# Kernel optimization log

Measured on AMD Instinct MI355X. Metric: run time of the kernel, lower is better.

Reference implementation:

```python
import jax, jax.numpy as jnp
import numpy as np
from jax import lax

BATCH, C, HH, WW = 4, 3, 512, 512


def _dark_min(x, patch):
    # min over channels, reflect-pad, min over patch x patch window (torch unfold+min)
    pad = (patch - 1) // 2
    m = jnp.min(x, axis=1, keepdims=True)                      # [B,1,H,W]
    m = jnp.pad(m, ((0, 0), (0, 0), (pad, pad), (pad, pad)), mode='reflect')
    return lax.reduce_window(m, jnp.array(jnp.inf, m.dtype), lax.min,
                             (1, 1, patch, patch), (1, 1, 1, 1), 'VALID')


def _soft_thresh(x, lam):
    return jnp.sign(x) * jnp.maximum(jnp.abs(x) - lam, 0.0)


def _conv3x3(x, w):
    return lax.conv_general_dilated(x, w, (1, 1), 'SAME',
                                    dimension_numbers=('NCHW', 'OIHW', 'NCHW'))


def setup_inputs() -> dict:
    key = jax.random.key(0)
    names = ['I', 't_p', 'B_p', 'B', 't', 'J', 'G', 'H', 'P', 'Q', 'u', 'v', 'X', 'Y']
    keys = jax.random.split(key, len(names) + 2)
    inp = {n: jax.random.uniform(keys[i], (BATCH, C, HH, WW), dtype=jnp.float32)
           for i, n in enumerate(names)}
    for g in ['gamma_1', 'gamma_2', 'gamma_3', 'gamma_4', 'gamma_5']:
        inp[g] = jnp.array([3.001], dtype=jnp.float32)
    inp['t1d_w'] = jax.random.normal(keys[-2], (1, 3, 1, 1), dtype=jnp.float32) * 0.3
    inp['hnet_w'] = jax.random.normal(keys[-1], (3, 3, 3, 3), dtype=jnp.float32) * 0.1
    inp['patch_size'] = 35
    return inp


def _forward(I, t_p, B_p, B, t, J, G, H, P, Q, u, v, X, Y,
             gamma_1, gamma_2, gamma_3, gamma_4, gamma_5, t1d_w, hnet_w, patch_size):
    lam1, lam2, lam3, lam4, lam5 = 1.0, 0.7, 0.3, 1.0, 1.0

    # ---- get_mean_value + mapping_index (vectorized over batch) ----
    mean = jnp.mean(J, axis=(2, 3))                 # [B,3]
    idx = jnp.argsort(mean, axis=1)                 # ascending, like torch.sort
    ms = jnp.take_along_axis(mean, idx, axis=1)     # sorted means
    gather = lambda k: jnp.take_along_axis(J, idx[:, k][:, None, None, None], axis=1)
    J_l, J_m, J_s = gather(2), gather(1), gather(0)           # [B,1,H,W]
    bar = lambda k: ms[:, k][:, None, None, None]
    J_m = J_m + (bar(2) - bar(1)) * J_l
    J_s = J_s + (bar(2) - bar(0)) * J_l
    ch = jnp.arange(3)[None, :]                     # scatter channels back
    J = jnp.where((ch == idx[:, 1:2])[:, :, None, None], J_m, J)
    J = jnp.where((ch == idx[:, 0:1])[:, :, None, None], J_s, J)

    # ---- B update (spatial mean broadcast back) ----
    Bn = (lam3 * B_p - lam1 * (J * t - I) * (1.0 - t)) / (lam1 * (1.0 - t) ** 2 + lam3)
    Bn = jnp.mean(Bn, axis=(2, 3), keepdims=True) * jnp.ones_like(I)

    # ---- t update + 1x1 conv + channel replicate ----
    tn = (lam2 * t_p + gamma_4 * H - lam1 * (Bn - I) * (J - Bn) - X) / \
         (lam1 * (J - Bn) ** 2 + lam2 + gamma_4)
    t1 = jnp.einsum('oc,bchw->bohw', t1d_w[:, :, 0, 0], tn)   # [B,1,H,W]
    tn = jnp.concatenate([t1, t1, t1], axis=1)

    # ---- J, u, v updates ----
    Jn = (lam1 * (tn * (I - Bn * (1.0 - tn))) + gamma_3 * G + gamma_4 * u
          - gamma_5 * v - Y + gamma_5) / (lam1 * tn * tn + gamma_3 + gamma_4 + gamma_5)
    un = (gamma_1 * u + gamma_4 * Jn) / (gamma_1 + gamma_4)
    vn = (gamma_2 * v - gamma_5 * Jn + gamma_5) / (gamma_2 + gamma_5)

    # ---- H_Net (conv stand-in for RDN), dual updates ----
    Hn = _conv3x3(tn + X / gamma_4, hnet_w)
    Xn = X + gamma_4 * (tn - Hn)
    Yn = Y + gamma_3 * (Jn - G)

    # ---- dark channel + soft threshold ----
    M_u = _dark_min(un, patch_size)
    M_v = _dark_min(vn, patch_size)
    Pn = _soft_thresh(M_u, lam4 / gamma_1)
    Qn = _soft_thresh(M_v, lam5 / gamma_1)

    return (Bn, tn, Jn, G, Hn, Pn, Qn, un, vn, Xn, Yn, gamma_3)


def reference(I, t_p, B_p, B, t, J, G, H, P, Q, u, v, X, Y,
              gamma_1, gamma_2, gamma_3, gamma_4, gamma_5, t1d_w, hnet_w, patch_size):
    return _forward(I, t_p, B_p, B, t, J, G, H, P, Q, u, v, X, Y,
                    gamma_1, gamma_2, gamma_3, gamma_4, gamma_5, t1d_w, hnet_w, patch_size)
```

## Files before the change

kernel.cpp:

```cpp
#include <hip/hip_runtime.h>
#include <math.h>

#define Bn_ 4
#define W_ 512
#define H_ 512
#define HW_ 262144
#define CHW_ 786432
#define NPLANE 12
#define NCHUNK 32

#define O_Bn 0
#define O_tn 3145728
#define O_Jn 6291456
#define O_G  9437184
#define O_Hn 12582912
#define O_Pn 15728640
#define O_Qn 16777216
#define O_un 17825792
#define O_vn 20971520
#define O_Xn 24117248
#define O_Yn 27262976
#define O_g3 30408704

#define LAM1 1.0f
#define LAM2 0.7f
#define LAM3 0.3f

__device__ __forceinline__ float blockReduceSum256(float v) {
    #pragma unroll
    for (int off = 32; off; off >>= 1) v += __shfl_down(v, off, 64);
    __shared__ float s[4];
    int lane = threadIdx.x & 63, w = threadIdx.x >> 6;
    if (!lane) s[w] = v;
    __syncthreads();
    if (threadIdx.x == 0) v = s[0] + s[1] + s[2] + s[3];
    return v;
}

__global__ __launch_bounds__(256) void kSumJ(const float* __restrict__ J,
                                             float* __restrict__ sums) {
    int blk = blockIdx.x;
    int plane = blk >> 5, chunk = blk & 31;
    const float4* p = (const float4*)(J + (size_t)plane * HW_ + chunk * 8192);
    float s = 0.f;
    #pragma unroll
    for (int k = 0; k < 8; ++k) {
        float4 v = p[threadIdx.x + k * 256];
        s += (v.x + v.y) + (v.z + v.w);
    }
    s = blockReduceSum256(s);
    if (threadIdx.x == 0) sums[blk] = s;
}

__global__ void kFinalizeJ(const float* __restrict__ sums,
                           float* __restrict__ alpha, int* __restrict__ idx2,
                           const float* __restrict__ g3p, float* __restrict__ outg3) {
    __shared__ float mean[12];
    int t = threadIdx.x;
    if (t < 12) {
        float s = 0.f;
        for (int k = 0; k < 32; ++k) s += sums[t * 32 + k];
        mean[t] = s * (1.0f / (float)HW_);
    }
    __syncthreads();
    if (t < 4) {
        float m0 = mean[t * 3 + 0], m1 = mean[t * 3 + 1], m2 = mean[t * 3 + 2];
        float m[3] = {m0, m1, m2};
        int r[3];
        #pragma unroll
        for (int i = 0; i < 3; ++i) {
            int ri = 0;
            #pragma unroll
            for (int j = 0; j < 3; ++j)
                if (j != i && (m[j] < m[i] || (m[j] == m[i] && j < i))) ri++;
            r[i] = ri;
        }
        int idx[3]; float ms[3];
        #pragma unroll
        for (int i = 0; i < 3; ++i) { idx[r[i]] = i; ms[r[i]] = m[i]; }
        idx2[t] = idx[2];
        float a[3] = {0.f, 0.f, 0.f};
        a[idx[1]] = ms[2] - ms[1];
        a[idx[0]] = ms[2] - ms[0];
        #pragma unroll
        for (int c = 0; c < 3; ++c) alpha[t * 3 + c] = a[c];
    }
    if (t == 0) *outg3 = g3p[0];
}

__global__ __launch_bounds__(256) void kSumB(const float* __restrict__ J,
                                             const float* __restrict__ tt,
                                             const float* __restrict__ B_p,
                                             const float* __restrict__ I,
                                             const float* __restrict__ alpha,
                                             const int* __restrict__ idx2,
                                             float* __restrict__ sums) {
    int blk = blockIdx.x;
    int plane = blk >> 5, chunk = blk & 31;
    int b = plane / 3;
    float al = alpha[plane];
    size_t base = (size_t)plane * HW_ + chunk * 8192;
    size_t lbase = (size_t)(b * 3 + idx2[b]) * HW_ + chunk * 8192;
    const float4* Jp  = (const float4*)(J + base);
    const float4* Jlp = (const float4*)(J + lbase);
    const float4* tp  = (const float4*)(tt + base);
    const float4* Bp  = (const float4*)(B_p + base);
    const float4* Ip  = (const float4*)(I + base);
    float s = 0.f;
    #pragma unroll 4
    for (int k = 0; k < 8; ++k) {
        int o = threadIdx.x + k * 256;
        float4 j = Jp[o], jl = Jlp[o], tv = tp[o], bp = Bp[o], iv = Ip[o];
        float jm, omt;
        jm = j.x + al * jl.x; omt = 1.f - tv.x;
        s += (LAM3 * bp.x - (jm * tv.x - iv.x) * omt) / (omt * omt + LAM3);
        jm = j.y + al * jl.y; omt = 1.f - tv.y;
        s += (LAM3 * bp.y - (jm * tv.y - iv.y) * omt) / (omt * omt + LAM3);
        jm = j.z + al * jl.z; omt = 1.f - tv.z;
        s += (LAM3 * bp.z - (jm * tv.z - iv.z) * omt) / (omt * omt + LAM3);
        jm = j.w + al * jl.w; omt = 1.f - tv.w;
        s += (LAM3 * bp.w - (jm * tv.w - iv.w) * omt) / (omt * omt + LAM3);
    }
    s = blockReduceSum256(s);
    if (threadIdx.x == 0) sums[blk] = s;
}

__global__ void kFinalizeB(const float* __restrict__ sums, float* __restrict__ BnS) {
    int t = threadIdx.x;
    if (t < 12) {
        float s = 0.f;
        for (int k = 0; k < 32; ++k) s += sums[t * 32 + k];
        BnS[t] = s * (1.0f / (float)HW_);
    }
}

__global__ __launch_bounds__(256) void kMain(
    const float* __restrict__ I, const float* __restrict__ t_p,
    const float* __restrict__ Hm, const float* __restrict__ Xm,
    const float* __restrict__ J, const float* __restrict__ u,
    const float* __restrict__ v, const float* __restrict__ Y,
    const float* __restrict__ G,
    const float* __restrict__ g1p, const float* __restrict__ g2p,
    const float* __restrict__ g3p, const float* __restrict__ g4p,
    const float* __restrict__ g5p, const float* __restrict__ t1w,
    const float* __restrict__ alpha, const int* __restrict__ idx2,
    const float* __restrict__ BnS,
    float* __restrict__ out)
{
    int id = blockIdx.x * 256 + threadIdx.x;
    int b = id >> 18, p = id & (HW_ - 1);
    float g1 = g1p[0], g2 = g2p[0], g3 = g3p[0], g4 = g4p[0], g5 = g5p[0];
    float wc0 = t1w[0], wc1 = t1w[1], wc2 = t1w[2];
    int i2 = idx2[b];
    float Jl = J[(size_t)(b * 3 + i2) * HW_ + p];

    float Iv[3], Bv[3], uv[3], vv[3], Yv[3], Gv[3];
    float wc[3] = {wc0, wc1, wc2};
    float t1 = 0.f;
    #pragma unroll
    for (int c = 0; c < 3; ++c) {
        size_t o = (size_t)(b * 3 + c) * HW_ + p;
        float Ic = I[o], tpc = t_p[o], Hc = Hm[o], Xc = Xm[o], Jc = J[o];
        float Jm = Jc + alpha[b * 3 + c] * Jl;
        float Bnv = BnS[b * 3 + c];
        float d = Jm - Bnv;
        float tnr = (LAM2 * tpc + g4 * Hc - (Bnv - Ic) * d - Xc) /
                    (d * d + LAM2 + g4);
        t1 += wc[c] * tnr;
        Iv[c] = Ic; Bv[c] = Bnv;
        uv[c] = u[o]; vv[c] = v[o]; Yv[c] = Y[o]; Gv[c] = G[o];
    }
    float cu = 1e30f, cv = 1e30f;
    float invDenJ = 1.f / (t1 * t1 + g3 + g4 + g5);
    float invDu = 1.f / (g1 + g4), invDv = 1.f / (g2 + g5);
    #pragma unroll
    for (int c = 0; c < 3; ++c) {
        size_t o = (size_t)(b * 3 + c) * HW_ + p;
        float Jn = (t1 * (Iv[c] - Bv[c] * (1.f - t1)) + g3 * Gv[c] + g4 * uv[c]
                    - g5 * vv[c] - Yv[c] + g5) * invDenJ;
        float un = (g1 * uv[c] + g4 * Jn) * invDu;
        float vn = (g2 * vv[c] - g5 * Jn + g5) * invDv;
        out[O_Bn + o] = Bv[c];
        out[O_tn + o] = t1;
        out[O_Jn + o] = Jn;
        out[O_G  + o] = Gv[c];
        out[O_un + o] = un;
        out[O_vn + o] = vn;
        out[O_Yn + o] = Yv[c] + g3 * (Jn - Gv[c]);
        cu = fminf(cu, un); cv = fminf(cv, vn);
    }
    out[O_Pn + b * HW_ + p] = cu;
    out[O_Qn + b * HW_ + p] = cv;
}

__global__ __launch_bounds__(256) void kHMin(float* __restrict__ out) {
    __shared__ float row[546];
    int blk = blockIdx.x;
    int tensor = blk >> 11;
    int rem = blk & 2047;
    int b = rem >> 9, y = rem & 511;
    const float* src = out + (tensor ? O_Qn : O_Pn) + b * HW_ + y * W_;
    float* dst = out + (tensor ? O_Xn : O_Hn) + b * HW_ + y * W_;
    for (int j = threadIdx.x; j < 546; j += 256) {
        int xx = j - 17;
        xx = xx < 0 ? -xx : (xx >= W_ ? 2 * W_ - 2 - xx : xx);
        row[j] = src[xx];
    }
    __syncthreads();
    for (int x = threadIdx.x; x < W_; x += 256) {
        float m = row[x];
        #pragma unroll
        for (int k = 1; k < 35; ++k) m = fminf(m, row[x + k]);
        dst[x] = m;
    }
}

__global__ __launch_bounds__(256) void kVMin(const float* __restrict__ g1p,
                                             float* __restrict__ out) {
    int tensor = blockIdx.x >> 12;
    int lid = ((blockIdx.x & 4095) << 8) + threadIdx.x;
    int b = lid >> 18, p = lid & (HW_ - 1);
    int y = p >> 9, x = p & 511;
    const float* R = out + (tensor ? O_Xn : O_Hn) + b * HW_;
    float m = 1e30f;
    #pragma unroll
    for (int k = 0; k < 35; ++k) {
        int yy = y + k - 17;
        yy = yy < 0 ? -yy : (yy >= H_ ? 2 * H_ - 2 - yy : yy);
        m = fminf(m, R[yy * W_ + x]);
    }
    float lam = 1.0f / g1p[0];
    float s = (m > 0.f) ? 1.f : (m < 0.f ? -1.f : 0.f);
    float r = s * fmaxf(fabsf(m) - lam, 0.f);
    out[(tensor ? O_Qn : O_Pn) + b * HW_ + p] = r;
}

__global__ __launch_bounds__(256) void kConv(const float* __restrict__ Xm,
                                             const float* __restrict__ hw,
                                             const float* __restrict__ g4p,
                                             float* __restrict__ out) {
    __shared__ float w[81];
    if (threadIdx.x < 81) w[threadIdx.x] = hw[threadIdx.x];
    __syncthreads();
    int id = blockIdx.x * 256 + threadIdx.x;
    int b = id >> 18, p = id & (HW_ - 1);
    int y = p >> 9, x = p & 511;
    float g4 = g4p[0], ig4 = 1.f / g4;
    const float* tn = out + O_tn + (size_t)b * CHW_;
    float acc0 = 0.f, acc1 = 0.f, acc2 = 0.f;
    #pragma unroll
    for (int ky = 0; ky < 3; ++ky) {
        int yy = y + ky - 1;
        if (yy < 0 || yy >= H_) continue;
        #pragma unroll
        for (int kx = 0; kx < 3; ++kx) {
            int xx = x + kx - 1;
            if (xx < 0 || xx >= W_) continue;
            int pp = yy * W_ + xx;
            float t1v = tn[pp];
            #pragma unroll
            for (int i = 0; i < 3; ++i) {
                float Av = t1v + Xm[(size_t)(b * 3 + i) * HW_ + pp] * ig4;
                int kk = i * 9 + ky * 3 + kx;
                acc0 += w[kk] * Av;
                acc1 += w[27 + kk] * Av;
                acc2 += w[54 + kk] * Av;
            }
        }
    }
    float t1c = tn[p];
    float acc[3] = {acc0, acc1, acc2};
    #pragma unroll
    for (int o = 0; o < 3; ++o) {
        size_t oo = (size_t)(b * 3 + o) * HW_ + p;
        out[O_Hn + oo] = acc[o];
        out[O_Xn + oo] = Xm[oo] + g4 * (t1c - acc[o]);
    }
}

extern "C" void kernel_launch(void* const* d_in, const int* in_sizes, int n_in,
                              void* d_out, int out_size, void* d_ws, size_t ws_size,
                              hipStream_t stream) {
    (void)in_sizes; (void)n_in; (void)out_size; (void)ws_size;
    const float* I   = (const float*)d_in[0];
    const float* t_p = (const float*)d_in[1];
    const float* B_p = (const float*)d_in[2];
    const float* tt  = (const float*)d_in[4];
    const float* J   = (const float*)d_in[5];
    const float* G   = (const float*)d_in[6];
    const float* Hm  = (const float*)d_in[7];
    const float* u   = (const float*)d_in[10];
    const float* v   = (const float*)d_in[11];
    const float* X   = (const float*)d_in[12];
    const float* Y   = (const float*)d_in[13];
    const float* g1  = (const float*)d_in[14];
    const float* g2  = (const float*)d_in[15];
    const float* g3  = (const float*)d_in[16];
    const float* g4  = (const float*)d_in[17];
    const float* g5  = (const float*)d_in[18];
    const float* t1w = (const float*)d_in[19];
    const float* hw  = (const float*)d_in[20];
    float* out = (float*)d_out;
    float* ws  = (float*)d_ws;

    float* sumJ  = ws;
    float* sumB  = ws + 384;
    float* alpha = ws + 768;
    int*   idx2  = (int*)(ws + 784);
    float* BnS   = ws + 788;

    kSumJ<<<384, 256, 0, stream>>>(J, sumJ);
    kFinalizeJ<<<1, 64, 0, stream>>>(sumJ, alpha, idx2, g3, out + O_g3);
    kSumB<<<384, 256, 0, stream>>>(J, tt, B_p, I, alpha, idx2, sumB);
    kFinalizeB<<<1, 64, 0, stream>>>(sumB, BnS);
    kMain<<<4096, 256, 0, stream>>>(I, t_p, Hm, X, J, u, v, Y, G,
                                    g1, g2, g3, g4, g5, t1w, alpha, idx2, BnS, out);
    kHMin<<<4096, 256, 0, stream>>>(out);
    kVMin<<<8192, 256, 0, stream>>>(g1, out);
    kConv<<<4096, 256, 0, stream>>>(X, hw, g4, out);
}
```

Measured before the change: 331.1 us.

## Merge mean and B reductions into one pass via linear decomposition; vectorize main kernel

The B estimate depends linearly on the channel-sorted J mixing coefficient. The two dependent reduction passes (J means, then B sums using alpha) are therefore replaced by a single pass that accumulates the J sums, base B sums and 9 cross terms, and the finalize step reconstructs BnS algebraically. This removes one full read of J, t, B_p and I plus two kernel launches. The main elementwise kernel is also rewritten to process float4 per thread. The trade-off is more registers and accumulators per thread in the reduction, and a small floating-point reassociation in BnS.

```diff
diff --git a/kernel.cpp b/kernel.cpp
--- a/kernel.cpp
+++ b/kernel.cpp
@@ -1,13 +1,11 @@
 #include <hip/hip_runtime.h>
 #include <math.h>
 
-#define Bn_ 4
 #define W_ 512
 #define H_ 512
 #define HW_ 262144
+#define HW4_ 65536
 #define CHW_ 786432
-#define NPLANE 12
-#define NCHUNK 32
 
 #define O_Bn 0
 #define O_tn 3145728
@@ -22,50 +20,92 @@
 #define O_Yn 27262976
 #define O_g3 30408704
 
-#define LAM1 1.0f
 #define LAM2 0.7f
 #define LAM3 0.3f
 
-__device__ __forceinline__ float blockReduceSum256(float v) {
-    #pragma unroll
-    for (int off = 32; off; off >>= 1) v += __shfl_down(v, off, 64);
-    __shared__ float s[4];
+__global__ __launch_bounds__(256) void kRed(const float* __restrict__ J,
+                                            const float* __restrict__ tt,
+                                            const float* __restrict__ B_p,
+                                            const float* __restrict__ I,
+                                            float* __restrict__ sums) {
+    int blk = blockIdx.x;
+    int b = blk >> 7, chunk = blk & 127;
+    size_t pb = (size_t)b * (CHW_ / 4);
+    size_t cb = (size_t)chunk * 512;
+    const float4* J4 = (const float4*)J;
+    const float4* t4 = (const float4*)tt;
+    const float4* B4 = (const float4*)B_p;
+    const float4* I4 = (const float4*)I;
+
+    float aJ[3] = {0.f, 0.f, 0.f};
+    float a1[3] = {0.f, 0.f, 0.f};
+    float a2[9] = {0.f, 0.f, 0.f, 0.f, 0.f, 0.f, 0.f, 0.f, 0.f};
+
+    #pragma unroll
+    for (int k = 0; k < 2; ++k) {
+        size_t o = cb + threadIdx.x + k * 256;
+        float4 j0 = J4[pb + 0 * HW4_ + o];
+        float4 j1 = J4[pb + 1 * HW4_ + o];
+        float4 j2 = J4[pb + 2 * HW4_ + o];
+        #pragma unroll
+        for (int c = 0; c < 3; ++c) {
+            float4 tv = t4[pb + (size_t)c * HW4_ + o];
+            float4 bp = B4[pb + (size_t)c * HW4_ + o];
+            float4 iv = I4[pb + (size_t)c * HW4_ + o];
+            float4 jc = (c == 0) ? j0 : (c == 1 ? j1 : j2);
+#define REDC(m) { \
+            float omt = 1.f - tv.m; \
+            float r = 1.f / (omt * omt + LAM3); \
+            float g = tv.m * omt * r; \
+            aJ[c] += jc.m; \
+            a1[c] += (LAM3 * bp.m - (jc.m * tv.m - iv.m) * omt) * r; \
+            a2[0 * 3 + c] += j0.m * g; \
+            a2[1 * 3 + c] += j1.m * g; \
+            a2[2 * 3 + c] += j2.m * g; }
+            REDC(x) REDC(y) REDC(z) REDC(w)
+#undef REDC
+        }
+    }
+
+    float vals[15];
+    #pragma unroll
+    for (int c = 0; c < 3; ++c) { vals[c] = aJ[c]; vals[3 + c] = a1[c]; }
+    #pragma unroll
+    for (int s = 0; s < 9; ++s) vals[6 + s] = a2[s];
+
+    __shared__ float lds[4][15];
     int lane = threadIdx.x & 63, w = threadIdx.x >> 6;
-    if (!lane) s[w] = v;
+    #pragma unroll
+    for (int s = 0; s < 15; ++s) {
+        float v = vals[s];
+        #pragma unroll
+        for (int off = 32; off; off >>= 1) v += __shfl_down(v, off, 64);
+        if (lane == 0) lds[w][s] = v;
+    }
     __syncthreads();
-    if (threadIdx.x == 0) v = s[0] + s[1] + s[2] + s[3];
-    return v;
-}
-
-__global__ __launch_bounds__(256) void kSumJ(const float* __restrict__ J,
-                                             float* __restrict__ sums) {
-    int blk = blockIdx.x;
-    int plane = blk >> 5, chunk = blk & 31;
-    const float4* p = (const float4*)(J + (size_t)plane * HW_ + chunk * 8192);
-    float s = 0.f;
-    #pragma unroll
-    for (int k = 0; k < 8; ++k) {
-        float4 v = p[threadIdx.x + k * 256];
-        s += (v.x + v.y) + (v.z + v.w);
-    }
-    s = blockReduceSum256(s);
-    if (threadIdx.x == 0) sums[blk] = s;
-}
-
-__global__ void kFinalizeJ(const float* __restrict__ sums,
-                           float* __restrict__ alpha, int* __restrict__ idx2,
-                           const float* __restrict__ g3p, float* __restrict__ outg3) {
-    __shared__ float mean[12];
+    if (threadIdx.x < 15) {
+        int s = threadIdx.x;
+        sums[blk * 16 + s] = lds[0][s] + lds[1][s] + lds[2][s] + lds[3][s];
+    }
+}
+
+__global__ void kFin(const float* __restrict__ sums,
+                     float* __restrict__ alpha, int* __restrict__ idx2,
+                     float* __restrict__ BnS,
+                     const float* __restrict__ g3p, float* __restrict__ outg3) {
+    __shared__ float tot[4][15];
     int t = threadIdx.x;
-    if (t < 12) {
-        float s = 0.f;
-        for (int k = 0; k < 32; ++k) s += sums[t * 32 + k];
-        mean[t] = s * (1.0f / (float)HW_);
+    if (t < 60) {
+        int b = t / 15, s = t % 15;
+        const float* p = sums + (size_t)b * 128 * 16 + s;
+        float acc = 0.f;
+        for (int ch = 0; ch < 128; ++ch) acc += p[ch * 16];
+        tot[b][s] = acc;
     }
     __syncthreads();
     if (t < 4) {
-        float m0 = mean[t * 3 + 0], m1 = mean[t * 3 + 1], m2 = mean[t * 3 + 2];
-        float m[3] = {m0, m1, m2};
+        const float invHW = 1.0f / (float)HW_;
+        float m[3] = {tot[t][0] * invHW, tot[t][1] * invHW, tot[t][2] * invHW};
         int r[3];
         #pragma unroll
         for (int i = 0; i < 3; ++i) {
@@ -83,55 +123,12 @@
         a[idx[1]] = ms[2] - ms[1];
         a[idx[0]] = ms[2] - ms[0];
         #pragma unroll
-        for (int c = 0; c < 3; ++c) alpha[t * 3 + c] = a[c];
+        for (int c = 0; c < 3; ++c) {
+            alpha[t * 3 + c] = a[c];
+            BnS[t * 3 + c] = (tot[t][3 + c] - a[c] * tot[t][6 + idx[2] * 3 + c]) * invHW;
+        }
     }
     if (t == 0) *outg3 = g3p[0];
-}
-
-__global__ __launch_bounds__(256) void kSumB(const float* __restrict__ J,
-                                             const float* __restrict__ tt,
-                                             const float* __restrict__ B_p,
-                                             const float* __restrict__ I,
-                                             const float* __restrict__ alpha,
-                                             const int* __restrict__ idx2,
-                                             float* __restrict__ sums) {
-    int blk = blockIdx.x;
-    int plane = blk >> 5, chunk = blk & 31;
-    int b = plane / 3;
-    float al = alpha[plane];
-    size_t base = (size_t)plane * HW_ + chunk * 8192;
-    size_t lbase = (size_t)(b * 3 + idx2[b]) * HW_ + chunk * 8192;
-    const float4* Jp  = (const float4*)(J + base);
-    const float4* Jlp = (const float4*)(J + lbase);
-    const float4* tp  = (const float4*)(tt + base);
-    const float4* Bp  = (const float4*)(B_p + base);
-    const float4* Ip  = (const float4*)(I + base);
-    float s = 0.f;
-    #pragma unroll 4
-    for (int k = 0; k < 8; ++k) {
-        int o = threadIdx.x + k * 256;
-        float4 j = Jp[o], jl = Jlp[o], tv = tp[o], bp = Bp[o], iv = Ip[o];
-        float jm, omt;
-        jm = j.x + al * jl.x; omt = 1.f - tv.x;
-        s += (LAM3 * bp.x - (jm * tv.x - iv.x) * omt) / (omt * omt + LAM3);
-        jm = j.y + al * jl.y; omt = 1.f - tv.y;
-        s += (LAM3 * bp.y - (jm * tv.y - iv.y) * omt) / (omt * omt + LAM3);
-        jm = j.z + al * jl.z; omt = 1.f - tv.z;
-        s += (LAM3 * bp.z - (jm * tv.z - iv.z) * omt) / (omt * omt + LAM3);
-        jm = j.w + al * jl.w; omt = 1.f - tv.w;
-        s += (LAM3 * bp.w - (jm * tv.w - iv.w) * omt) / (omt * omt + LAM3);
-    }
-    s = blockReduceSum256(s);
-    if (threadIdx.x == 0) sums[blk] = s;
-}
-
-__global__ void kFinalizeB(const float* __restrict__ sums, float* __restrict__ BnS) {
-    int t = threadIdx.x;
-    if (t < 12) {
-        float s = 0.f;
-        for (int k = 0; k < 32; ++k) s += sums[t * 32 + k];
-        BnS[t] = s * (1.0f / (float)HW_);
-    }
 }
 
 __global__ __launch_bounds__(256) void kMain(
@@ -148,49 +145,75 @@
     float* __restrict__ out)
 {
     int id = blockIdx.x * 256 + threadIdx.x;
-    int b = id >> 18, p = id & (HW_ - 1);
+    int b = id >> 16, q = id & (HW4_ - 1);
     float g1 = g1p[0], g2 = g2p[0], g3 = g3p[0], g4 = g4p[0], g5 = g5p[0];
-    float wc0 = t1w[0], wc1 = t1w[1], wc2 = t1w[2];
+    float wc[3] = {t1w[0], t1w[1], t1w[2]};
     int i2 = idx2[b];
-    float Jl = J[(size_t)(b * 3 + i2) * HW_ + p];
-
-    float Iv[3], Bv[3], uv[3], vv[3], Yv[3], Gv[3];
-    float wc[3] = {wc0, wc1, wc2};
-    float t1 = 0.f;
+    size_t pb = (size_t)b * (CHW_ / 4);
+    const float4* I4p = (const float4*)I;
+    const float4* tp4p = (const float4*)t_p;
+    const float4* H4p = (const float4*)Hm;
+    const float4* X4p = (const float4*)Xm;
+    const float4* J4p = (const float4*)J;
+    const float4* u4p = (const float4*)u;
+    const float4* v4p = (const float4*)v;
+    const float4* Y4p = (const float4*)Y;
+    const float4* G4p = (const float4*)G;
+    float4* o4 = (float4*)out;
+
+    float4 Jl = J4p[pb + (size_t)i2 * HW4_ + q];
+    float4 t1 = make_float4(0.f, 0.f, 0.f, 0.f);
+    float4 Isv[3]; float Bsv[3];
+    const float den2 = LAM2 + g4;
     #pragma unroll
     for (int c = 0; c < 3; ++c) {
-        size_t o = (size_t)(b * 3 + c) * HW_ + p;
-        float Ic = I[o], tpc = t_p[o], Hc = Hm[o], Xc = Xm[o], Jc = J[o];
-        float Jm = Jc + alpha[b * 3 + c] * Jl;
-        float Bnv = BnS[b * 3 + c];
-        float d = Jm - Bnv;
-        float tnr = (LAM2 * tpc + g4 * Hc - (Bnv - Ic) * d - Xc) /
-                    (d * d + LAM2 + g4);
-        t1 += wc[c] * tnr;
-        Iv[c] = Ic; Bv[c] = Bnv;
-        uv[c] = u[o]; vv[c] = v[o]; Yv[c] = Y[o]; Gv[c] = G[o];
-    }
-    float cu = 1e30f, cv = 1e30f;
-    float invDenJ = 1.f / (t1 * t1 + g3 + g4 + g5);
+        size_t o = pb + (size_t)c * HW4_ + q;
+        float4 I4 = I4p[o], tp4 = tp4p[o], H4 = H4p[o], X4 = X4p[o], Jv = J4p[o];
+        float al = alpha[b * 3 + c], Bnv = BnS[b * 3 + c];
+        float wcc = wc[c];
+#define STEP1(m) { \
+        float d_ = (Jv.m + al * Jl.m) - Bnv; \
+        float tnr_ = (LAM2 * tp4.m + g4 * H4.m - (Bnv - I4.m) * d_ - X4.m) / (d_ * d_ + den2); \
+        t1.m += wcc * tnr_; }
+        STEP1(x) STEP1(y) STEP1(z) STEP1(w)
+#undef STEP1
+        Isv[c] = I4; Bsv[c] = Bnv;
+    }
+    float g345 = g3 + g4 + g5;
+    float4 invDen;
+    invDen.x = 1.f / (t1.x * t1.x + g345);
+    invDen.y = 1.f / (t1.y * t1.y + g345);
+    invDen.z = 1.f / (t1.z * t1.z + g345);
+    invDen.w = 1.f / (t1.w * t1.w + g345);
     float invDu = 1.f / (g1 + g4), invDv = 1.f / (g2 + g5);
+    float4 cu = make_float4(1e30f, 1e30f, 1e30f, 1e30f);
+    float4 cv = cu;
     #pragma unroll
     for (int c = 0; c < 3; ++c) {
-        size_t o = (size_t)(b * 3 + c) * HW_ + p;
-        float Jn = (t1 * (Iv[c] - Bv[c] * (1.f - t1)) + g3 * Gv[c] + g4 * uv[c]
-                    - g5 * vv[c] - Yv[c] + g5) * invDenJ;
-        float un = (g1 * uv[c] + g4 * Jn) * invDu;
-        float vn = (g2 * vv[c] - g5 * Jn + g5) * invDv;
-        out[O_Bn + o] = Bv[c];
-        out[O_tn + o] = t1;
-        out[O_Jn + o] = Jn;
-        out[O_G  + o] = Gv[c];
-        out[O_un + o] = un;
-        out[O_vn + o] = vn;
-        out[O_Yn + o] = Yv[c] + g3 * (Jn - Gv[c]);
-        cu = fminf(cu, un); cv = fminf(cv, vn);
-    }
-    out[O_Pn + b * HW_ + p] = cu;
-    out[O_Qn + b * HW_ + p] = cv;
+        size_t o = pb + (size_t)c * HW4_ + q;
+        float4 u4 = u4p[o], v4 = v4p[o], Y4 = Y4p[o], G4 = G4p[o];
+        float Bnv = Bsv[c];
+        float4 Jn4, un4, vn4, Yn4;
+#define STEP2(m) { \
+        float Jn_ = (t1.m * (Isv[c].m - Bnv * (1.f - t1.m)) + g3 * G4.m + g4 * u4.m \
+                     - g5 * v4.m - Y4.m + g5) * invDen.m; \
+        float un_ = (g1 * u4.m + g4 * Jn_) * invDu; \
+        float vn_ = (g2 * v4.m - g5 * Jn_ + g5) * invDv; \
+        Jn4.m = Jn_; un4.m = un_; vn4.m = vn_; \
+        Yn4.m = Y4.m + g3 * (Jn_ - G4.m); \
+        cu.m = fminf(cu.m, un_); cv.m = fminf(cv.m, vn_); }
+        STEP2(x) STEP2(y) STEP2(z) STEP2(w)
+#undef STEP2
+        o4[O_Bn / 4 + o] = make_float4(Bnv, Bnv, Bnv, Bnv);
+        o4[O_tn / 4 + o] = t1;
+        o4[O_Jn / 4 + o] = Jn4;
+        o4[O_G  / 4 + o] = G4;
+        o4[O_un / 4 + o] = un4;
+        o4[O_vn / 4 + o] = vn4;
+        o4[O_Yn / 4 + o] = Yn4;
+    }
+    o4[O_Pn / 4 + (size_t)b * HW4_ + q] = cu;
+    o4[O_Qn / 4 + (size_t)b * HW4_ + q] = cv;
 }
 
 __global__ __launch_bounds__(256) void kHMin(float* __restrict__ out) {
@@ -303,17 +326,14 @@
     float* out = (float*)d_out;
     float* ws  = (float*)d_ws;
 
-    float* sumJ  = ws;
-    float* sumB  = ws + 384;
-    float* alpha = ws + 768;
-    int*   idx2  = (int*)(ws + 784);
-    float* BnS   = ws + 788;
-
-    kSumJ<<<384, 256, 0, stream>>>(J, sumJ);
-    kFinalizeJ<<<1, 64, 0, stream>>>(sumJ, alpha, idx2, g3, out + O_g3);
-    kSumB<<<384, 256, 0, stream>>>(J, tt, B_p, I, alpha, idx2, sumB);
-    kFinalizeB<<<1, 64, 0, stream>>>(sumB, BnS);
-    kMain<<<4096, 256, 0, stream>>>(I, t_p, Hm, X, J, u, v, Y, G,
+    float* sums  = ws;
+    float* alpha = ws + 8192;
+    int*   idx2  = (int*)(ws + 8204);
+    float* BnS   = ws + 8208;
+
+    kRed<<<512, 256, 0, stream>>>(J, tt, B_p, I, sums);
+    kFin<<<1, 64, 0, stream>>>(sums, alpha, idx2, BnS, g3, out + O_g3);
+    kMain<<<1024, 256, 0, stream>>>(I, t_p, Hm, X, J, u, v, Y, G,
                                     g1, g2, g3, g4, g5, t1w, alpha, idx2, BnS, out);
     kHMin<<<4096, 256, 0, stream>>>(out);
     kVMin<<<8192, 256, 0, stream>>>(g1, out);
```

After: 329.2 us. About the same (-0.6%).
